# Optimization experiments

Hardware: AMD Instinct MI355X
Metric: run time of the kernel (lower is better)

Reference implementation:

```python
import jax, jax.numpy as jnp
import numpy as np

B, N, D_IN, H, NH = 8, 1024, 3072, 128, 4
DH = H // NH
LN_EPS = 1e-5


def make_mask(key, p):
    A = jax.random.bernoulli(key, p, (N, N)).astype(jnp.float32)
    A_tilde = A + jnp.eye(N, dtype=jnp.float32)  # add self-loops
    return jnp.where(A_tilde > 0, 0.0, -jnp.inf).astype(jnp.float32)


def setup_inputs() -> dict:
    key = jax.random.key(0)
    ks = jax.random.split(key, 20)
    s = 0.02
    inp = {
        "stim_features": jax.random.normal(ks[0], (B, D_IN), jnp.float32),
        # stim encoder
        "W_enc1": jax.random.normal(ks[1], (2 * H, D_IN), jnp.float32) * s,
        "b_enc1": jnp.zeros((2 * H,), jnp.float32),
        "ln_g": jnp.ones((2 * H,), jnp.float32),
        "ln_b": jnp.zeros((2 * H,), jnp.float32),
        "W_enc2": jax.random.normal(ks[2], (H, 2 * H), jnp.float32) * s,
        "b_enc2": jnp.zeros((H,), jnp.float32),
        "voxel_emb": jax.random.normal(ks[3], (N, H), jnp.float32) * 0.01,
        # GAT projection weights (Linear, no bias), [out, in]
        "W_func1": jax.random.normal(ks[4], (H, H), jnp.float32) * s,
        "W_roi1": jax.random.normal(ks[5], (H, H), jnp.float32) * s,
        "W_func2": jax.random.normal(ks[6], (H, H), jnp.float32) * s,
        "W_roi2": jax.random.normal(ks[7], (H, H), jnp.float32) * s,
        # fusion / skip / readout
        "W_fu1": jax.random.normal(ks[8], (H, 2 * H), jnp.float32) * s,
        "b_fu1": jnp.zeros((H,), jnp.float32),
        "W_fu2": jax.random.normal(ks[9], (H, 2 * H), jnp.float32) * s,
        "b_fu2": jnp.zeros((H,), jnp.float32),
        "W_sk1": jax.random.normal(ks[10], (H, H), jnp.float32) * s,
        "b_sk1": jnp.zeros((H,), jnp.float32),
        "W_sk2": jax.random.normal(ks[11], (H, H), jnp.float32) * s,
        "b_sk2": jnp.zeros((H,), jnp.float32),
        "W_ro": jax.random.normal(ks[12], (1, H), jnp.float32) * s,
        "b_ro": jnp.zeros((1,), jnp.float32),
        # static adjacency masks (buffers, 0 / -inf)
        "mask_func": make_mask(ks[13], 0.01),
        "mask_roi": make_mask(ks[14], 0.05),
    }
    return inp


def gat(h, W, mask):
    # h: [B, N, H]; W: [H, H]; mask: [N, N]
    Bq, Nq, _ = h.shape
    Wh = (h @ W.T).reshape(Bq, Nq, NH, DH).transpose(0, 2, 1, 3)  # [B, nh, N, dh]
    scores = jnp.einsum("bhnd,bhmd->bhnm", Wh, Wh) / np.sqrt(DH)
    scores = scores + mask[None, None]
    attn = jax.nn.softmax(scores, axis=-1)  # dropout = identity (eval mode)
    hp = jnp.einsum("bhnm,bhmd->bhnd", attn, Wh)
    hp = hp.transpose(0, 2, 1, 3).reshape(Bq, Nq, NH * DH)
    return jax.nn.elu(hp)


def reference(stim_features, W_enc1, b_enc1, ln_g, ln_b, W_enc2, b_enc2,
              voxel_emb, W_func1, W_roi1, W_func2, W_roi2,
              W_fu1, b_fu1, W_fu2, b_fu2, W_sk1, b_sk1, W_sk2, b_sk2,
              W_ro, b_ro, mask_func, mask_roi):
    # stim encoder: Linear -> LayerNorm -> GELU -> Linear (dropout = identity)
    z = stim_features @ W_enc1.T + b_enc1
    mu = jnp.mean(z, axis=-1, keepdims=True)
    var = jnp.var(z, axis=-1, keepdims=True)
    z = (z - mu) * jax.lax.rsqrt(var + LN_EPS) * ln_g + ln_b
    z = jax.nn.gelu(z, approximate=False)
    g = z @ W_enc2.T + b_enc2  # [B, H]

    x = g[:, None, :] + voxel_emb[None]  # [B, N, H]
    x_res1 = x
    h1 = jnp.concatenate([gat(x, W_func1, mask_func), gat(x, W_roi1, mask_roi)], axis=-1)
    x = h1 @ W_fu1.T + b_fu1
    x = x + (x_res1 @ W_sk1.T + b_sk1)
    x_res2 = x
    h2 = jnp.concatenate([gat(x, W_func2, mask_func), gat(x, W_roi2, mask_roi)], axis=-1)
    x = h2 @ W_fu2.T + b_fu2
    x = x + (x_res2 @ W_sk2.T + b_sk2)
    pred = (x @ W_ro.T + b_ro)[..., 0]  # [B, N]
    return pred
```

## Files before the change

kernel.cpp:

```cpp
#include <hip/hip_runtime.h>
#include <hip/hip_bf16.h>
#include <math.h>

#define B_SZ 8
#define N_SZ 1024
#define D_IN 3072
#define H_SZ 128
#define NH 4
#define DH 32
#define TWO_H 256
#define LN_EPS 1e-5f
#define CAP 128

typedef __attribute__((ext_vector_type(8))) short bf16x8;
typedef __attribute__((ext_vector_type(8))) unsigned short u16x8;
typedef __attribute__((ext_vector_type(4))) float f32x4;
typedef __attribute__((ext_vector_type(4))) unsigned int u32x4;

__device__ inline unsigned short f2bf(float f) {
    unsigned int u = __builtin_bit_cast(unsigned int, f);
    u += 0x7fffu + ((u >> 16) & 1u);
    return (unsigned short)(u >> 16);
}

__global__ __launch_bounds__(256) void prep_kernel(
        const float* __restrict__ Wfu1, const float* __restrict__ Wsk1,
        const float* __restrict__ Wfu2, const float* __restrict__ Wsk2,
        const float* __restrict__ Wf1, const float* __restrict__ Wr1,
        const float* __restrict__ Wf2, const float* __restrict__ Wr2,
        unsigned short* __restrict__ wb,
        const float* __restrict__ m0, const float* __restrict__ m1,
        int* __restrict__ i0, int* __restrict__ i1,
        int* __restrict__ d0, int* __restrict__ d1,
        const float* __restrict__ stim, const float* __restrict__ W1,
        const float* __restrict__ b1, float* __restrict__ z) {
    const int bid = blockIdx.x;
    const int tid = threadIdx.x;

    if (bid < 128) {
        const int j = bid;
        wb[j * 384 + tid] = f2bf(Wfu1[j * 256 + tid]);
        wb[49152 + j * 384 + tid] = f2bf(Wfu2[j * 256 + tid]);
        if (tid < 128) {
            wb[j * 384 + 256 + tid]         = f2bf(Wsk1[j * 128 + tid]);
            wb[49152 + j * 384 + 256 + tid] = f2bf(Wsk2[j * 128 + tid]);
            wb[98304  + j * 128 + tid] = f2bf(Wf1[j * 128 + tid]);
            wb[114688 + j * 128 + tid] = f2bf(Wr1[j * 128 + tid]);
            wb[131072 + j * 128 + tid] = f2bf(Wf2[j * 128 + tid]);
            wb[147456 + j * 128 + tid] = f2bf(Wr2[j * 128 + tid]);
        }
    } else if (bid < 640) {
        const int bIdx = bid - 128;
        const int gsel = bIdx >> 8;
        const float* mask = gsel ? m1 : m0;
        int* idx = gsel ? i1 : i0;
        int* deg = gsel ? d1 : d0;
        const int row = (bIdx & 255) * 4 + (tid >> 6);
        const int lane = tid & 63;
        const float* mrow = mask + (size_t)row * N_SZ;
        int* irow = idx + (size_t)row * CAP;

        int base = 0;
        #pragma unroll 4
        for (int t = 0; t < N_SZ / 64; ++t) {
            int c = t * 64 + lane;
            bool edge = (mrow[c] == 0.0f);
            unsigned long long ball = __ballot(edge);
            unsigned long long below = ball & ((1ull << lane) - 1ull);
            if (edge) {
                int p = base + __popcll(below);
                if (p < CAP) irow[p] = c;
            }
            base += __popcll(ball);
        }
        if (lane == 0) deg[row] = (base < CAP) ? base : CAP;
    } else {
        const int j = bid - 640;
        const float4* w4 = (const float4*)(W1 + (size_t)j * D_IN);
        const float4* s4 = (const float4*)stim;

        float acc[B_SZ];
        #pragma unroll
        for (int b = 0; b < B_SZ; ++b) acc[b] = 0.0f;

        #pragma unroll
        for (int i = 0; i < D_IN / 4 / 256; ++i) {
            const int k4 = tid + i * 256;
            const float4 w = w4[k4];
            #pragma unroll
            for (int b = 0; b < B_SZ; ++b) {
                const float4 s = s4[b * (D_IN / 4) + k4];
                acc[b] += s.x * w.x + s.y * w.y + s.z * w.z + s.w * w.w;
            }
        }
        #pragma unroll
        for (int b = 0; b < B_SZ; ++b) {
            float v = acc[b];
            v += __shfl_xor(v, 1);  v += __shfl_xor(v, 2);  v += __shfl_xor(v, 4);
            v += __shfl_xor(v, 8);  v += __shfl_xor(v, 16); v += __shfl_xor(v, 32);
            acc[b] = v;
        }
        __shared__ float red[4][B_SZ];
        const int wave = tid >> 6, lane = tid & 63;
        if (lane == 0) {
            #pragma unroll
            for (int b = 0; b < B_SZ; ++b) red[wave][b] = acc[b];
        }
        __syncthreads();
        if (tid < B_SZ) {
            float v = red[0][tid] + red[1][tid] + red[2][tid] + red[3][tid];
            z[tid * TWO_H + j] = v + b1[j];
        }
    }
}

__global__ __launch_bounds__(256) void enc23_kernel(
        const float* __restrict__ z,
        const float* __restrict__ lng, const float* __restrict__ lnb,
        const float* __restrict__ W2, const float* __restrict__ b2,
        float* __restrict__ g) {
    __shared__ float red[TWO_H];
    __shared__ float zgs[TWO_H];
    __shared__ float gp[2][H_SZ];
    const int b = blockIdx.x;
    const int tid = threadIdx.x;

    float zi = z[b * TWO_H + tid];
    red[tid] = zi; __syncthreads();
    for (int s = 128; s > 0; s >>= 1) { if (tid < s) red[tid] += red[tid + s]; __syncthreads(); }
    float mu = red[0] * (1.0f / TWO_H);
    __syncthreads();
    float dz = zi - mu;
    red[tid] = dz * dz; __syncthreads();
    for (int s = 128; s > 0; s >>= 1) { if (tid < s) red[tid] += red[tid + s]; __syncthreads(); }
    float var = red[0] * (1.0f / TWO_H);

    float zn = dz * (1.0f / sqrtf(var + LN_EPS)) * lng[tid] + lnb[tid];
    zgs[tid] = 0.5f * zn * (1.0f + erff(zn * 0.70710678118654752f));
    __syncthreads();

    const int j = tid & 127, half = tid >> 7;
    const float* w2r = W2 + (size_t)j * TWO_H + half * 128;
    const float* zh = &zgs[half * 128];
    float s = 0.0f;
    #pragma unroll 4
    for (int k = 0; k < 128; ++k) s += zh[k] * w2r[k];
    gp[half][j] = s;
    __syncthreads();
    if (tid < H_SZ) g[b * H_SZ + tid] = gp[0][tid] + gp[1][tid] + b2[tid];
}

template<int NSEG, bool OB16, bool AEMB, bool RO, bool AB16>
__global__ __launch_bounds__(256) void gemm_mfma(
        const void* __restrict__ a0, const void* __restrict__ a1,
        const void* __restrict__ a2,
        const float* __restrict__ gvec, const float* __restrict__ emb,
        const unsigned short* __restrict__ wba, const unsigned short* __restrict__ wbb,
        const float* __restrict__ bias1, const float* __restrict__ bias2,
        void* __restrict__ outa, void* __restrict__ outb,
        const float* __restrict__ Wro, const float* __restrict__ bro,
        float* __restrict__ pred) {
    const unsigned short* wb = blockIdx.y ? wbb : wba;
    void* out = blockIdx.y ? outb : outa;
    const int KW = NSEG * 128;

    __shared__ __align__(16) short As[32 * 128];
    __shared__ __align__(16) short Bs[64 * 128];
    __shared__ float part[2][32];

    const int bid = blockIdx.x;
    const int ct = bid & 1, rt = bid >> 1;
    const int row0 = rt * 32, col0 = ct * 64;
    const int tid = threadIdx.x;
    const int lane = tid & 63, w = tid >> 6;
    const int wm = w >> 1, wn = w & 1;
    const int lrow = lane & 15, lk = lane >> 4;

    f32x4 acc0 = {0.f, 0.f, 0.f, 0.f};
    f32x4 acc1 = {0.f, 0.f, 0.f, 0.f};

    for (int seg = 0; seg < NSEG; ++seg) {
        const void* src = (seg == 0) ? a0 : ((seg == 1) ? a1 : a2);
        const bool useEmb = AEMB && (NSEG == 1 || seg == 2);
        if (seg) __syncthreads();
        for (int gi = tid; gi < 512; gi += 256) {
            const int r = gi >> 4, kq = gi & 15;
            u16x8 t;
            if (useEmb) {
                const int row = row0 + r;
                const float4* gp = (const float4*)(gvec + (size_t)(row >> 10) * H_SZ) + kq * 2;
                const float4* ep = (const float4*)(emb + (size_t)(row & 1023) * H_SZ) + kq * 2;
                const float4 g0 = gp[0], g1 = gp[1], e0 = ep[0], e1 = ep[1];
                t[0] = f2bf(g0.x + e0.x); t[1] = f2bf(g0.y + e0.y);
                t[2] = f2bf(g0.z + e0.z); t[3] = f2bf(g0.w + e0.w);
                t[4] = f2bf(g1.x + e1.x); t[5] = f2bf(g1.y + e1.y);
                t[6] = f2bf(g1.z + e1.z); t[7] = f2bf(g1.w + e1.w);
            } else if (AB16) {
                t = *(const u16x8*)((const unsigned short*)src
                                    + (size_t)(row0 + r) * H_SZ + kq * 8);
            } else {
                const float4* sp = (const float4*)((const float*)src
                                    + (size_t)(row0 + r) * H_SZ) + kq * 2;
                const float4 v0 = sp[0], v1 = sp[1];
                t[0] = f2bf(v0.x); t[1] = f2bf(v0.y); t[2] = f2bf(v0.z); t[3] = f2bf(v0.w);
                t[4] = f2bf(v1.x); t[5] = f2bf(v1.y); t[6] = f2bf(v1.z); t[7] = f2bf(v1.w);
            }
            *(u16x8*)&As[r * 128 + ((kq * 8) ^ ((r & 7) << 3))] = t;
        }
        for (int gi = tid; gi < 1024; gi += 256) {
            const int c = gi >> 4, kq = gi & 15;
            const float4 v = *(const float4*)(wb + (size_t)(col0 + c) * KW + seg * 128 + kq * 8);
            *(float4*)&Bs[c * 128 + ((kq * 8) ^ ((c & 7) << 3))] = v;
        }
        __syncthreads();

        #pragma unroll
        for (int ks = 0; ks < 4; ++ks) {
            const int kof = ks * 32 + lk * 8;
            const int r = wm * 16 + lrow;
            const bf16x8 a = *(const bf16x8*)&As[r * 128 + (kof ^ ((r & 7) << 3))];
            const int c0 = wn * 32 + lrow;
            const bf16x8 b0 = *(const bf16x8*)&Bs[c0 * 128 + (kof ^ ((c0 & 7) << 3))];
            const int c1 = c0 + 16;
            const bf16x8 b1 = *(const bf16x8*)&Bs[c1 * 128 + (kof ^ ((c1 & 7) << 3))];
            acc0 = __builtin_amdgcn_mfma_f32_16x16x32_bf16(a, b0, acc0, 0, 0, 0);
            acc1 = __builtin_amdgcn_mfma_f32_16x16x32_bf16(a, b1, acc1, 0, 0, 0);
        }
    }

    const int rb = row0 + wm * 16 + lk * 4;
    if constexpr (RO) {
        float pr[4] = {0.f, 0.f, 0.f, 0.f};
        #pragma unroll
        for (int fc = 0; fc < 2; ++fc) {
            const int c = col0 + wn * 32 + fc * 16 + lrow;
            const float bias = bias1[c] + bias2[c];
            const float wro = Wro[c];
            const f32x4 a = fc ? acc1 : acc0;
            #pragma unroll
            for (int rr = 0; rr < 4; ++rr) pr[rr] += (a[rr] + bias) * wro;
        }
        #pragma unroll
        for (int rr = 0; rr < 4; ++rr) {
            pr[rr] += __shfl_xor(pr[rr], 1);
            pr[rr] += __shfl_xor(pr[rr], 2);
            pr[rr] += __shfl_xor(pr[rr], 4);
            pr[rr] += __shfl_xor(pr[rr], 8);
        }
        if (lrow == 0) {
            #pragma unroll
            for (int rr = 0; rr < 4; ++rr) part[wn][wm * 16 + lk * 4 + rr] = pr[rr];
        }
        __syncthreads();
        if (tid < 32) {
            float v = part[0][tid] + part[1][tid];
            if (ct == 0) v += bro[0];
            atomicAdd(pred + row0 + tid, v);
        }
    } else {
        #pragma unroll
        for (int fc = 0; fc < 2; ++fc) {
            const int c = col0 + wn * 32 + fc * 16 + lrow;
            const float bias = (bias1 ? bias1[c] : 0.0f) + (bias2 ? bias2[c] : 0.0f);
            const f32x4 a = fc ? acc1 : acc0;
            #pragma unroll
            for (int rr = 0; rr < 4; ++rr) {
                if constexpr (OB16) {
                    ((unsigned short*)out)[(size_t)(rb + rr) * H_SZ + c] = f2bf(a[rr] + bias);
                } else {
                    ((float*)out)[(size_t)(rb + rr) * H_SZ + c] = a[rr] + bias;
                }
            }
        }
    }
}

__global__ __launch_bounds__(256) void fusproj_kernel(
        const unsigned short* __restrict__ hf, const unsigned short* __restrict__ hr,
        const float* __restrict__ gvec, const float* __restrict__ emb,
        const unsigned short* __restrict__ wcat,
        const float* __restrict__ bfu, const float* __restrict__ bsk,
        const unsigned short* __restrict__ wpf, const unsigned short* __restrict__ wpr,
        unsigned short* __restrict__ x2, unsigned short* __restrict__ whf,
        unsigned short* __restrict__ whr) {
    __shared__ __align__(16) short As[16 * 128];
    __shared__ __align__(16) short Bs[128 * 128];
    const int row0 = blockIdx.x * 16;
    const int tid = threadIdx.x;
    const int lane = tid & 63, w = tid >> 6;
    const int lrow = lane & 15, lk = lane >> 4;

    f32x4 acc0 = {0.f, 0.f, 0.f, 0.f};
    f32x4 acc1 = {0.f, 0.f, 0.f, 0.f};

    for (int seg = 0; seg < 3; ++seg) {
        if (seg) __syncthreads();
        {
            const int r = tid >> 4, kq = tid & 15;
            u16x8 t;
            if (seg == 0) {
                t = *(const u16x8*)(hf + (size_t)(row0 + r) * H_SZ + kq * 8);
            } else if (seg == 1) {
                t = *(const u16x8*)(hr + (size_t)(row0 + r) * H_SZ + kq * 8);
            } else {
                const int row = row0 + r;
                const float4* gp = (const float4*)(gvec + (size_t)(row >> 10) * H_SZ) + kq * 2;
                const float4* ep = (const float4*)(emb + (size_t)(row & 1023) * H_SZ) + kq * 2;
                const float4 g0 = gp[0], g1 = gp[1], e0 = ep[0], e1 = ep[1];
                t[0] = f2bf(g0.x + e0.x); t[1] = f2bf(g0.y + e0.y);
                t[2] = f2bf(g0.z + e0.z); t[3] = f2bf(g0.w + e0.w);
                t[4] = f2bf(g1.x + e1.x); t[5] = f2bf(g1.y + e1.y);
                t[6] = f2bf(g1.z + e1.z); t[7] = f2bf(g1.w + e1.w);
            }
            *(u16x8*)&As[r * 128 + ((kq * 8) ^ ((r & 7) << 3))] = t;
        }
        for (int gi = tid; gi < 2048; gi += 256) {
            const int c = gi >> 4, kq = gi & 15;
            const float4 v = *(const float4*)(wcat + (size_t)c * 384 + seg * 128 + kq * 8);
            *(float4*)&Bs[c * 128 + ((kq * 8) ^ ((c & 7) << 3))] = v;
        }
        __syncthreads();

        #pragma unroll
        for (int ks = 0; ks < 4; ++ks) {
            const int kof = ks * 32 + lk * 8;
            const bf16x8 a = *(const bf16x8*)&As[lrow * 128 + (kof ^ ((lrow & 7) << 3))];
            const int c0 = w * 32 + lrow;
            const bf16x8 b0 = *(const bf16x8*)&Bs[c0 * 128 + (kof ^ ((c0 & 7) << 3))];
            const int c1 = c0 + 16;
            const bf16x8 b1 = *(const bf16x8*)&Bs[c1 * 128 + (kof ^ ((c1 & 7) << 3))];
            acc0 = __builtin_amdgcn_mfma_f32_16x16x32_bf16(a, b0, acc0, 0, 0, 0);
            acc1 = __builtin_amdgcn_mfma_f32_16x16x32_bf16(a, b1, acc1, 0, 0, 0);
        }
    }
    __syncthreads();

    const int rb = lk * 4;
    #pragma unroll
    for (int fc = 0; fc < 2; ++fc) {
        const int c = w * 32 + fc * 16 + lrow;
        const float bias = bfu[c] + bsk[c];
        const f32x4 a = fc ? acc1 : acc0;
        #pragma unroll
        for (int rr = 0; rr < 4; ++rr) {
            const unsigned short v = f2bf(a[rr] + bias);
            x2[(size_t)(row0 + rb + rr) * H_SZ + c] = v;
            const int rl = rb + rr;
            As[rl * 128 + (((c & ~7) ^ ((rl & 7) << 3)) | (c & 7))] = (short)v;
        }
    }
    __syncthreads();

    #pragma unroll
    for (int gsel = 0; gsel < 2; ++gsel) {
        const unsigned short* wp = gsel ? wpr : wpf;
        unsigned short* out = gsel ? whr : whf;
        if (gsel) __syncthreads();
        for (int gi = tid; gi < 2048; gi += 256) {
            const int c = gi >> 4, kq = gi & 15;
            const float4 v = *(const float4*)(wp + (size_t)c * 128 + kq * 8);
            *(float4*)&Bs[c * 128 + ((kq * 8) ^ ((c & 7) << 3))] = v;
        }
        __syncthreads();
        f32x4 p0 = {0.f, 0.f, 0.f, 0.f};
        f32x4 p1 = {0.f, 0.f, 0.f, 0.f};
        #pragma unroll
        for (int ks = 0; ks < 4; ++ks) {
            const int kof = ks * 32 + lk * 8;
            const bf16x8 a = *(const bf16x8*)&As[lrow * 128 + (kof ^ ((lrow & 7) << 3))];
            const int c0 = w * 32 + lrow;
            const bf16x8 b0 = *(const bf16x8*)&Bs[c0 * 128 + (kof ^ ((c0 & 7) << 3))];
            const int c1 = c0 + 16;
            const bf16x8 b1 = *(const bf16x8*)&Bs[c1 * 128 + (kof ^ ((c1 & 7) << 3))];
            p0 = __builtin_amdgcn_mfma_f32_16x16x32_bf16(a, b0, p0, 0, 0, 0);
            p1 = __builtin_amdgcn_mfma_f32_16x16x32_bf16(a, b1, p1, 0, 0, 0);
        }
        #pragma unroll
        for (int fc = 0; fc < 2; ++fc) {
            const int c = w * 32 + fc * 16 + lrow;
            const f32x4 a = fc ? p1 : p0;
            #pragma unroll
            for (int rr = 0; rr < 4; ++rr)
                out[(size_t)(row0 + rb + rr) * H_SZ + c] = f2bf(a[rr]);
        }
    }
}

__global__ __launch_bounds__(256) void fusro_kernel(
        const unsigned short* __restrict__ hf, const unsigned short* __restrict__ hr,
        const unsigned short* __restrict__ x2,
        const unsigned short* __restrict__ wcat,
        const float* __restrict__ bfu, const float* __restrict__ bsk,
        const float* __restrict__ Wro, const float* __restrict__ bro,
        float* __restrict__ pred) {
    __shared__ __align__(16) short As[16 * 128];
    __shared__ __align__(16) short Bs[128 * 128];
    __shared__ float part[4][16];
    const int row0 = blockIdx.x * 16;
    const int tid = threadIdx.x;
    const int lane = tid & 63, w = tid >> 6;
    const int lrow = lane & 15, lk = lane >> 4;

    f32x4 acc0 = {0.f, 0.f, 0.f, 0.f};
    f32x4 acc1 = {0.f, 0.f, 0.f, 0.f};

    for (int seg = 0; seg < 3; ++seg) {
        if (seg) __syncthreads();
        {
            const int r = tid >> 4, kq = tid & 15;
            const unsigned short* src = (seg == 0) ? hf : ((seg == 1) ? hr : x2);
            const u16x8 t = *(const u16x8*)(src + (size_t)(row0 + r) * H_SZ + kq * 8);
            *(u16x8*)&As[r * 128 + ((kq * 8) ^ ((r & 7) << 3))] = t;
        }
        for (int gi = tid; gi < 2048; gi += 256) {
            const int c = gi >> 4, kq = gi & 15;
            const float4 v = *(const float4*)(wcat + (size_t)c * 384 + seg * 128 + kq * 8);
            *(float4*)&Bs[c * 128 + ((kq * 8) ^ ((c & 7) << 3))] = v;
        }
        __syncthreads();

        #pragma unroll
        for (int ks = 0; ks < 4; ++ks) {
            const int kof = ks * 32 + lk * 8;
            const bf16x8 a = *(const bf16x8*)&As[lrow * 128 + (kof ^ ((lrow & 7) << 3))];
            const int c0 = w * 32 + lrow;
            const bf16x8 b0 = *(const bf16x8*)&Bs[c0 * 128 + (kof ^ ((c0 & 7) << 3))];
            const int c1 = c0 + 16;
            const bf16x8 b1 = *(const bf16x8*)&Bs[c1 * 128 + (kof ^ ((c1 & 7) << 3))];
            acc0 = __builtin_amdgcn_mfma_f32_16x16x32_bf16(a, b0, acc0, 0, 0, 0);
            acc1 = __builtin_amdgcn_mfma_f32_16x16x32_bf16(a, b1, acc1, 0, 0, 0);
        }
    }

    const int rb = lk * 4;
    float pr[4] = {0.f, 0.f, 0.f, 0.f};
    #pragma unroll
    for (int fc = 0; fc < 2; ++fc) {
        const int c = w * 32 + fc * 16 + lrow;
        const float bias = bfu[c] + bsk[c];
        const float wro = Wro[c];
        const f32x4 a = fc ? acc1 : acc0;
        #pragma unroll
        for (int rr = 0; rr < 4; ++rr) pr[rr] += (a[rr] + bias) * wro;
    }
    #pragma unroll
    for (int rr = 0; rr < 4; ++rr) {
        pr[rr] += __shfl_xor(pr[rr], 1);
        pr[rr] += __shfl_xor(pr[rr], 2);
        pr[rr] += __shfl_xor(pr[rr], 4);
        pr[rr] += __shfl_xor(pr[rr], 8);
    }
    if (lrow == 0) {
        #pragma unroll
        for (int rr = 0; rr < 4; ++rr) part[w][rb + rr] = pr[rr];
    }
    __syncthreads();
    if (tid < 16)
        pred[row0 + tid] = part[0][tid] + part[1][tid] + part[2][tid] + part[3][tid] + bro[0];
}

__global__ __launch_bounds__(256) void attn_kernel(
        const unsigned short* __restrict__ Wha, const unsigned short* __restrict__ Whb,
        const int* __restrict__ ia, const int* __restrict__ ib,
        const int* __restrict__ da, const int* __restrict__ db,
        unsigned short* __restrict__ oa, unsigned short* __restrict__ ob) {
    const unsigned short* Wh = blockIdx.y ? Whb : Wha;
    const int* idx = blockIdx.y ? ib : ia;
    const int* deg = blockIdx.y ? db : da;
    unsigned short* out = blockIdx.y ? ob : oa;

    const int bid = blockIdx.x;
    const int b = bid & 7;
    const int i = ((bid >> 3) << 2) | (threadIdx.x >> 6);
    const int bi = b * N_SZ + i;
    const int lane = threadIdx.x & 63;
    const int c = lane & 15;
    const int e4 = lane >> 4;

    const u32x4 qb = *(const u32x4*)(Wh + (size_t)bi * H_SZ + c * 8);
    float qf[8];
    #pragma unroll
    for (int m = 0; m < 4; ++m) {
        qf[2 * m]     = __builtin_bit_cast(float, qb[m] << 16) * 0.25505654741110714f;
        qf[2 * m + 1] = __builtin_bit_cast(float, qb[m] & 0xffff0000u) * 0.25505654741110714f;
    }

    const int dg = deg[i];
    const int* row = idx + (size_t)i * CAP;
    int idxv0 = row[lane] & 1023;
    int idxv1 = (dg > 64) ? (row[64 + lane] & 1023) : 0;

    const unsigned short* kbase = Wh + (size_t)b * N_SZ * H_SZ;

    float acc[8];
    #pragma unroll
    for (int k = 0; k < 8; ++k) acc[k] = 0.0f;
    float l = 0.0f;

    auto loadSeg = [&](int s, u32x4* kv) {
        const int srcv = (s >= 4) ? idxv1 : idxv0;
        const int off16 = (s & 3) << 4;
        #pragma unroll
        for (int t = 0; t < 4; ++t) {
            const int j0 = __builtin_amdgcn_readlane(srcv, off16 + 4 * t);
            const int j1 = __builtin_amdgcn_readlane(srcv, off16 + 4 * t + 1);
            const int j2 = __builtin_amdgcn_readlane(srcv, off16 + 4 * t + 2);
            const int j3 = __builtin_amdgcn_readlane(srcv, off16 + 4 * t + 3);
            const int jlo = (e4 & 1) ? j1 : j0;
            const int jhi = (e4 & 1) ? j3 : j2;
            const int j = (e4 & 2) ? jhi : jlo;
            kv[t] = *(const u32x4*)(kbase + (size_t)j * H_SZ + c * 8);
        }
    };
    auto computeSeg = [&](int s, const u32x4* kv) {
        const int ebase = s << 4;
        #pragma unroll
        for (int t = 0; t < 4; ++t) {
            float kf[8];
            #pragma unroll
            for (int m = 0; m < 4; ++m) {
                kf[2 * m]     = __builtin_bit_cast(float, kv[t][m] << 16);
                kf[2 * m + 1] = __builtin_bit_cast(float, kv[t][m] & 0xffff0000u);
            }
            float s2 = 0.0f;
            #pragma unroll
            for (int k = 0; k < 8; ++k) s2 += qf[k] * kf[k];
            s2 += __shfl_xor(s2, 1);
            s2 += __shfl_xor(s2, 2);
            const bool valid = (ebase + 4 * t + e4) < dg;
            const float p = valid ? __builtin_amdgcn_exp2f(s2) : 0.0f;
            l += p;
            #pragma unroll
            for (int k = 0; k < 8; ++k) acc[k] += p * kf[k];
        }
    };

    const int nseg = (dg + 15) >> 4;
    u32x4 kvA[4], kvB[4];
    loadSeg(0, kvA);
    int seg = 0;
    while (true) {
        if (seg + 1 < nseg) loadSeg(seg + 1, kvB);
        computeSeg(seg, kvA);
        ++seg; if (seg >= nseg) break;
        if (seg + 1 < nseg) loadSeg(seg + 1, kvA);
        computeSeg(seg, kvB);
        ++seg; if (seg >= nseg) break;
    }

    l += __shfl_xor(l, 16);
    l += __shfl_xor(l, 32);
    #pragma unroll
    for (int k = 0; k < 8; ++k) {
        acc[k] += __shfl_xor(acc[k], 16);
        acc[k] += __shfl_xor(acc[k], 32);
    }

    if (e4 == 0) {
        const float inv = 1.0f / l;
        u16x8 ov;
        #pragma unroll
        for (int k = 0; k < 8; ++k) {
            const float hp = acc[k] * inv;
            const float o = (hp > 0.0f) ? hp
                 : (__builtin_amdgcn_exp2f(hp * 1.4426950408889634f) - 1.0f);
            ov[k] = f2bf(o);
        }
        *(u16x8*)(out + (size_t)bi * H_SZ + c * 8) = ov;
    }
}

extern "C" void kernel_launch(void* const* d_in, const int* in_sizes, int n_in,
                              void* d_out, int out_size, void* d_ws, size_t ws_size,
                              hipStream_t stream) {
    const float* stim   = (const float*)d_in[0];
    const float* W_enc1 = (const float*)d_in[1];
    const float* b_enc1 = (const float*)d_in[2];
    const float* ln_g   = (const float*)d_in[3];
    const float* ln_b   = (const float*)d_in[4];
    const float* W_enc2 = (const float*)d_in[5];
    const float* b_enc2 = (const float*)d_in[6];
    const float* vox    = (const float*)d_in[7];
    const float* W_f1   = (const float*)d_in[8];
    const float* W_r1   = (const float*)d_in[9];
    const float* W_f2   = (const float*)d_in[10];
    const float* W_r2   = (const float*)d_in[11];
    const float* W_fu1  = (const float*)d_in[12];
    const float* b_fu1  = (const float*)d_in[13];
    const float* W_fu2  = (const float*)d_in[14];
    const float* b_fu2  = (const float*)d_in[15];
    const float* W_sk1  = (const float*)d_in[16];
    const float* b_sk1  = (const float*)d_in[17];
    const float* W_sk2  = (const float*)d_in[18];
    const float* b_sk2  = (const float*)d_in[19];
    const float* W_ro   = (const float*)d_in[20];
    const float* b_ro   = (const float*)d_in[21];
    const float* mask_f = (const float*)d_in[22];
    const float* mask_r = (const float*)d_in[23];

    float* pred = (float*)d_out;

    float* ws  = (float*)d_ws;
    float* z   = ws;
    float* g   = z + 2048;
    unsigned short* x2_16 = (unsigned short*)(g + 1024);
    unsigned short* hf16  = x2_16 + 1048576;
    unsigned short* hr16  = hf16 + 1048576;
    unsigned short* Whf16 = hr16 + 1048576;
    unsigned short* Whr16 = Whf16 + 1048576;
    int* idxf  = (int*)(Whr16 + 1048576);
    int* idxr  = idxf + N_SZ * CAP;
    int* degf  = idxr + N_SZ * CAP;
    int* degr  = degf + N_SZ;
    unsigned short* wb16 = (unsigned short*)(degr + N_SZ);
    unsigned short* wcat1 = wb16;
    unsigned short* wcat2 = wb16 + 49152;
    unsigned short* wpf1  = wb16 + 98304;
    unsigned short* wpr1  = wb16 + 114688;
    unsigned short* wpf2  = wb16 + 131072;
    unsigned short* wpr2  = wb16 + 147456;

    const int BN = B_SZ * N_SZ;

    prep_kernel<<<896, 256, 0, stream>>>(
        W_fu1, W_sk1, W_fu2, W_sk2, W_f1, W_r1, W_f2, W_r2, wb16,
        mask_f, mask_r, idxf, idxr, degf, degr,
        stim, W_enc1, b_enc1, z);
    enc23_kernel<<<B_SZ, 256, 0, stream>>>(z, ln_g, ln_b, W_enc2, b_enc2, g);

    gemm_mfma<1, true, true, false, false><<<dim3(BN / 32 * 2, 2), 256, 0, stream>>>(
        nullptr, nullptr, nullptr, g, vox, wpf1, wpr1, nullptr, nullptr,
        Whf16, Whr16, nullptr, nullptr, nullptr);
    attn_kernel<<<dim3(BN / 4, 2), 256, 0, stream>>>(Whf16, Whr16, idxf, idxr, degf, degr,
                                                     hf16, hr16);
    fusproj_kernel<<<BN / 16, 256, 0, stream>>>(
        hf16, hr16, g, vox, wcat1, b_fu1, b_sk1, wpf2, wpr2,
        x2_16, Whf16, Whr16);

    attn_kernel<<<dim3(BN / 4, 2), 256, 0, stream>>>(Whf16, Whr16, idxf, idxr, degf, degr,
                                                     hf16, hr16);
    fusro_kernel<<<BN / 16, 256, 0, stream>>>(
        hf16, hr16, x2_16, wcat2, b_fu2, b_sk2, W_ro, b_ro, pred);
}
```

Measured before the change: 88.21 us.

## Double row tile in fusion kernels, skip padded neighbor loads, simplify gemm template

The fusproj and fusro kernels now process 32 rows per block instead of 16. Each wave computes two 16-row MFMA tiles against the same B fragments, so each 128x128 weight tile staged in shared memory is reused over twice as many rows and half as many blocks are launched. The attention kernel now skips neighbor gathers and compute for 4-element groups past the node degree in the final segment, avoiding wasted loads. The generic gemm template also drops its unused multi-segment, bias and readout paths. Halving the block count lowers parallelism and raises register use per wave.

```diff
diff --git a/kernel.cpp b/kernel.cpp
--- a/kernel.cpp
+++ b/kernel.cpp
@@ -150,23 +150,18 @@
     if (tid < H_SZ) g[b * H_SZ + tid] = gp[0][tid] + gp[1][tid] + b2[tid];
 }
 
-template<int NSEG, bool OB16, bool AEMB, bool RO, bool AB16>
+template<int NSEG, bool AEMB, bool AB16>
 __global__ __launch_bounds__(256) void gemm_mfma(
-        const void* __restrict__ a0, const void* __restrict__ a1,
-        const void* __restrict__ a2,
+        const void* __restrict__ a0,
         const float* __restrict__ gvec, const float* __restrict__ emb,
         const unsigned short* __restrict__ wba, const unsigned short* __restrict__ wbb,
-        const float* __restrict__ bias1, const float* __restrict__ bias2,
-        void* __restrict__ outa, void* __restrict__ outb,
-        const float* __restrict__ Wro, const float* __restrict__ bro,
-        float* __restrict__ pred) {
+        void* __restrict__ outa, void* __restrict__ outb) {
     const unsigned short* wb = blockIdx.y ? wbb : wba;
     void* out = blockIdx.y ? outb : outa;
     const int KW = NSEG * 128;
 
     __shared__ __align__(16) short As[32 * 128];
     __shared__ __align__(16) short Bs[64 * 128];
-    __shared__ float part[2][32];
 
     const int bid = blockIdx.x;
     const int ct = bid & 1, rt = bid >> 1;
@@ -180,13 +175,11 @@
     f32x4 acc1 = {0.f, 0.f, 0.f, 0.f};
 
     for (int seg = 0; seg < NSEG; ++seg) {
-        const void* src = (seg == 0) ? a0 : ((seg == 1) ? a1 : a2);
-        const bool useEmb = AEMB && (NSEG == 1 || seg == 2);
         if (seg) __syncthreads();
         for (int gi = tid; gi < 512; gi += 256) {
             const int r = gi >> 4, kq = gi & 15;
             u16x8 t;
-            if (useEmb) {
+            if (AEMB) {
                 const int row = row0 + r;
                 const float4* gp = (const float4*)(gvec + (size_t)(row >> 10) * H_SZ) + kq * 2;
                 const float4* ep = (const float4*)(emb + (size_t)(row & 1023) * H_SZ) + kq * 2;
@@ -196,10 +189,10 @@
                 t[4] = f2bf(g1.x + e1.x); t[5] = f2bf(g1.y + e1.y);
                 t[6] = f2bf(g1.z + e1.z); t[7] = f2bf(g1.w + e1.w);
             } else if (AB16) {
-                t = *(const u16x8*)((const unsigned short*)src
+                t = *(const u16x8*)((const unsigned short*)a0
                                     + (size_t)(row0 + r) * H_SZ + kq * 8);
             } else {
-                const float4* sp = (const float4*)((const float*)src
+                const float4* sp = (const float4*)((const float*)a0
                                     + (size_t)(row0 + r) * H_SZ) + kq * 2;
                 const float4 v0 = sp[0], v1 = sp[1];
                 t[0] = f2bf(v0.x); t[1] = f2bf(v0.y); t[2] = f2bf(v0.z); t[3] = f2bf(v0.w);
@@ -229,49 +222,13 @@
     }
 
     const int rb = row0 + wm * 16 + lk * 4;
-    if constexpr (RO) {
-        float pr[4] = {0.f, 0.f, 0.f, 0.f};
-        #pragma unroll
-        for (int fc = 0; fc < 2; ++fc) {
-            const int c = col0 + wn * 32 + fc * 16 + lrow;
-            const float bias = bias1[c] + bias2[c];
-            const float wro = Wro[c];
-            const f32x4 a = fc ? acc1 : acc0;
-            #pragma unroll
-            for (int rr = 0; rr < 4; ++rr) pr[rr] += (a[rr] + bias) * wro;
-        }
-        #pragma unroll
-        for (int rr = 0; rr < 4; ++rr) {
-            pr[rr] += __shfl_xor(pr[rr], 1);
-            pr[rr] += __shfl_xor(pr[rr], 2);
-            pr[rr] += __shfl_xor(pr[rr], 4);
-            pr[rr] += __shfl_xor(pr[rr], 8);
-        }
-        if (lrow == 0) {
-            #pragma unroll
-            for (int rr = 0; rr < 4; ++rr) part[wn][wm * 16 + lk * 4 + rr] = pr[rr];
-        }
-        __syncthreads();
-        if (tid < 32) {
-            float v = part[0][tid] + part[1][tid];
-            if (ct == 0) v += bro[0];
-            atomicAdd(pred + row0 + tid, v);
-        }
-    } else {
-        #pragma unroll
-        for (int fc = 0; fc < 2; ++fc) {
-            const int c = col0 + wn * 32 + fc * 16 + lrow;
-            const float bias = (bias1 ? bias1[c] : 0.0f) + (bias2 ? bias2[c] : 0.0f);
-            const f32x4 a = fc ? acc1 : acc0;
-            #pragma unroll
-            for (int rr = 0; rr < 4; ++rr) {
-                if constexpr (OB16) {
-                    ((unsigned short*)out)[(size_t)(rb + rr) * H_SZ + c] = f2bf(a[rr] + bias);
-                } else {
-                    ((float*)out)[(size_t)(rb + rr) * H_SZ + c] = a[rr] + bias;
-                }
-            }
-        }
+    #pragma unroll
+    for (int fc = 0; fc < 2; ++fc) {
+        const int c = col0 + wn * 32 + fc * 16 + lrow;
+        const f32x4 a = fc ? acc1 : acc0;
+        #pragma unroll
+        for (int rr = 0; rr < 4; ++rr)
+            ((unsigned short*)out)[(size_t)(rb + rr) * H_SZ + c] = f2bf(a[rr]);
     }
 }
 
@@ -283,20 +240,20 @@
         const unsigned short* __restrict__ wpf, const unsigned short* __restrict__ wpr,
         unsigned short* __restrict__ x2, unsigned short* __restrict__ whf,
         unsigned short* __restrict__ whr) {
-    __shared__ __align__(16) short As[16 * 128];
+    __shared__ __align__(16) short As[32 * 128];
     __shared__ __align__(16) short Bs[128 * 128];
-    const int row0 = blockIdx.x * 16;
+    const int row0 = blockIdx.x * 32;
     const int tid = threadIdx.x;
     const int lane = tid & 63, w = tid >> 6;
     const int lrow = lane & 15, lk = lane >> 4;
 
-    f32x4 acc0 = {0.f, 0.f, 0.f, 0.f};
-    f32x4 acc1 = {0.f, 0.f, 0.f, 0.f};
+    f32x4 acc[2][2] = {{{0.f,0.f,0.f,0.f},{0.f,0.f,0.f,0.f}},
+                       {{0.f,0.f,0.f,0.f},{0.f,0.f,0.f,0.f}}};
 
     for (int seg = 0; seg < 3; ++seg) {
         if (seg) __syncthreads();
-        {
-            const int r = tid >> 4, kq = tid & 15;
+        for (int gi = tid; gi < 512; gi += 256) {
+            const int r = gi >> 4, kq = gi & 15;
             u16x8 t;
             if (seg == 0) {
                 t = *(const u16x8*)(hf + (size_t)(row0 + r) * H_SZ + kq * 8);
@@ -324,29 +281,35 @@
         #pragma unroll
         for (int ks = 0; ks < 4; ++ks) {
             const int kof = ks * 32 + lk * 8;
-            const bf16x8 a = *(const bf16x8*)&As[lrow * 128 + (kof ^ ((lrow & 7) << 3))];
-            const int c0 = w * 32 + lrow;
+            const int c0 = w * 32 + lrow, c1 = c0 + 16;
             const bf16x8 b0 = *(const bf16x8*)&Bs[c0 * 128 + (kof ^ ((c0 & 7) << 3))];
-            const int c1 = c0 + 16;
             const bf16x8 b1 = *(const bf16x8*)&Bs[c1 * 128 + (kof ^ ((c1 & 7) << 3))];
-            acc0 = __builtin_amdgcn_mfma_f32_16x16x32_bf16(a, b0, acc0, 0, 0, 0);
-            acc1 = __builtin_amdgcn_mfma_f32_16x16x32_bf16(a, b1, acc1, 0, 0, 0);
+            #pragma unroll
+            for (int m = 0; m < 2; ++m) {
+                const int r = m * 16 + lrow;
+                const bf16x8 a = *(const bf16x8*)&As[r * 128 + (kof ^ ((r & 7) << 3))];
+                acc[m][0] = __builtin_amdgcn_mfma_f32_16x16x32_bf16(a, b0, acc[m][0], 0, 0, 0);
+                acc[m][1] = __builtin_amdgcn_mfma_f32_16x16x32_bf16(a, b1, acc[m][1], 0, 0, 0);
+            }
         }
     }
     __syncthreads();
 
-    const int rb = lk * 4;
     #pragma unroll
-    for (int fc = 0; fc < 2; ++fc) {
-        const int c = w * 32 + fc * 16 + lrow;
-        const float bias = bfu[c] + bsk[c];
-        const f32x4 a = fc ? acc1 : acc0;
-        #pragma unroll
-        for (int rr = 0; rr < 4; ++rr) {
-            const unsigned short v = f2bf(a[rr] + bias);
-            x2[(size_t)(row0 + rb + rr) * H_SZ + c] = v;
-            const int rl = rb + rr;
-            As[rl * 128 + (((c & ~7) ^ ((rl & 7) << 3)) | (c & 7))] = (short)v;
+    for (int m = 0; m < 2; ++m) {
+        const int rb = m * 16 + lk * 4;
+        #pragma unroll
+        for (int fc = 0; fc < 2; ++fc) {
+            const int c = w * 32 + fc * 16 + lrow;
+            const float bias = bfu[c] + bsk[c];
+            const f32x4 a = acc[m][fc];
+            #pragma unroll
+            for (int rr = 0; rr < 4; ++rr) {
+                const unsigned short v = f2bf(a[rr] + bias);
+                x2[(size_t)(row0 + rb + rr) * H_SZ + c] = v;
+                const int rl = rb + rr;
+                As[rl * 128 + (((c & ~7) ^ ((rl & 7) << 3)) | (c & 7))] = (short)v;
+            }
         }
     }
     __syncthreads();
@@ -362,26 +325,33 @@
             *(float4*)&Bs[c * 128 + ((kq * 8) ^ ((c & 7) << 3))] = v;
         }
         __syncthreads();
-        f32x4 p0 = {0.f, 0.f, 0.f, 0.f};
-        f32x4 p1 = {0.f, 0.f, 0.f, 0.f};
+        f32x4 p[2][2] = {{{0.f,0.f,0.f,0.f},{0.f,0.f,0.f,0.f}},
+                         {{0.f,0.f,0.f,0.f},{0.f,0.f,0.f,0.f}}};
         #pragma unroll
         for (int ks = 0; ks < 4; ++ks) {
             const int kof = ks * 32 + lk * 8;
-            const bf16x8 a = *(const bf16x8*)&As[lrow * 128 + (kof ^ ((lrow & 7) << 3))];
-            const int c0 = w * 32 + lrow;
+            const int c0 = w * 32 + lrow, c1 = c0 + 16;
             const bf16x8 b0 = *(const bf16x8*)&Bs[c0 * 128 + (kof ^ ((c0 & 7) << 3))];
-            const int c1 = c0 + 16;
             const bf16x8 b1 = *(const bf16x8*)&Bs[c1 * 128 + (kof ^ ((c1 & 7) << 3))];
-            p0 = __builtin_amdgcn_mfma_f32_16x16x32_bf16(a, b0, p0, 0, 0, 0);
-            p1 = __builtin_amdgcn_mfma_f32_16x16x32_bf16(a, b1, p1, 0, 0, 0);
-        }
-        #pragma unroll
-        for (int fc = 0; fc < 2; ++fc) {
-            const int c = w * 32 + fc * 16 + lrow;
-            const f32x4 a = fc ? p1 : p0;
-            #pragma unroll
-            for (int rr = 0; rr < 4; ++rr)
-                out[(size_t)(row0 + rb + rr) * H_SZ + c] = f2bf(a[rr]);
+            #pragma unroll
+            for (int m = 0; m < 2; ++m) {
+                const int r = m * 16 + lrow;
+                const bf16x8 a = *(const bf16x8*)&As[r * 128 + (kof ^ ((r & 7) << 3))];
+                p[m][0] = __builtin_amdgcn_mfma_f32_16x16x32_bf16(a, b0, p[m][0], 0, 0, 0);
+                p[m][1] = __builtin_amdgcn_mfma_f32_16x16x32_bf16(a, b1, p[m][1], 0, 0, 0);
+            }
+        }
+        #pragma unroll
+        for (int m = 0; m < 2; ++m) {
+            const int rb = m * 16 + lk * 4;
+            #pragma unroll
+            for (int fc = 0; fc < 2; ++fc) {
+                const int c = w * 32 + fc * 16 + lrow;
+                const f32x4 a = p[m][fc];
+                #pragma unroll
+                for (int rr = 0; rr < 4; ++rr)
+                    out[(size_t)(row0 + rb + rr) * H_SZ + c] = f2bf(a[rr]);
+            }
         }
     }
 }
@@ -393,21 +363,21 @@
         const float* __restrict__ bfu, const float* __restrict__ bsk,
         const float* __restrict__ Wro, const float* __restrict__ bro,
         float* __restrict__ pred) {
-    __shared__ __align__(16) short As[16 * 128];
+    __shared__ __align__(16) short As[32 * 128];
     __shared__ __align__(16) short Bs[128 * 128];
-    __shared__ float part[4][16];
-    const int row0 = blockIdx.x * 16;
+    __shared__ float part[4][32];
+    const int row0 = blockIdx.x * 32;
     const int tid = threadIdx.x;
     const int lane = tid & 63, w = tid >> 6;
     const int lrow = lane & 15, lk = lane >> 4;
 
-    f32x4 acc0 = {0.f, 0.f, 0.f, 0.f};
-    f32x4 acc1 = {0.f, 0.f, 0.f, 0.f};
+    f32x4 acc[2][2] = {{{0.f,0.f,0.f,0.f},{0.f,0.f,0.f,0.f}},
+                       {{0.f,0.f,0.f,0.f},{0.f,0.f,0.f,0.f}}};
 
     for (int seg = 0; seg < 3; ++seg) {
         if (seg) __syncthreads();
-        {
-            const int r = tid >> 4, kq = tid & 15;
+        for (int gi = tid; gi < 512; gi += 256) {
+            const int r = gi >> 4, kq = gi & 15;
             const unsigned short* src = (seg == 0) ? hf : ((seg == 1) ? hr : x2);
             const u16x8 t = *(const u16x8*)(src + (size_t)(row0 + r) * H_SZ + kq * 8);
             *(u16x8*)&As[r * 128 + ((kq * 8) ^ ((r & 7) << 3))] = t;
@@ -422,40 +392,46 @@
         #pragma unroll
         for (int ks = 0; ks < 4; ++ks) {
             const int kof = ks * 32 + lk * 8;
-            const bf16x8 a = *(const bf16x8*)&As[lrow * 128 + (kof ^ ((lrow & 7) << 3))];
-            const int c0 = w * 32 + lrow;
+            const int c0 = w * 32 + lrow, c1 = c0 + 16;
             const bf16x8 b0 = *(const bf16x8*)&Bs[c0 * 128 + (kof ^ ((c0 & 7) << 3))];
-            const int c1 = c0 + 16;
             const bf16x8 b1 = *(const bf16x8*)&Bs[c1 * 128 + (kof ^ ((c1 & 7) << 3))];
-            acc0 = __builtin_amdgcn_mfma_f32_16x16x32_bf16(a, b0, acc0, 0, 0, 0);
-            acc1 = __builtin_amdgcn_mfma_f32_16x16x32_bf16(a, b1, acc1, 0, 0, 0);
-        }
-    }
-
-    const int rb = lk * 4;
-    float pr[4] = {0.f, 0.f, 0.f, 0.f};
+            #pragma unroll
+            for (int m = 0; m < 2; ++m) {
+                const int r = m * 16 + lrow;
+                const bf16x8 a = *(const bf16x8*)&As[r * 128 + (kof ^ ((r & 7) << 3))];
+                acc[m][0] = __builtin_amdgcn_mfma_f32_16x16x32_bf16(a, b0, acc[m][0], 0, 0, 0);
+                acc[m][1] = __builtin_amdgcn_mfma_f32_16x16x32_bf16(a, b1, acc[m][1], 0, 0, 0);
+            }
+        }
+    }
+
     #pragma unroll
-    for (int fc = 0; fc < 2; ++fc) {
-        const int c = w * 32 + fc * 16 + lrow;
-        const float bias = bfu[c] + bsk[c];
-        const float wro = Wro[c];
-        const f32x4 a = fc ? acc1 : acc0;
-        #pragma unroll
-        for (int rr = 0; rr < 4; ++rr) pr[rr] += (a[rr] + bias) * wro;
-    }
-    #pragma unroll
-    for (int rr = 0; rr < 4; ++rr) {
-        pr[rr] += __shfl_xor(pr[rr], 1);
-        pr[rr] += __shfl_xor(pr[rr], 2);
-        pr[rr] += __shfl_xor(pr[rr], 4);
-        pr[rr] += __shfl_xor(pr[rr], 8);
-    }
-    if (lrow == 0) {
-        #pragma unroll
-        for (int rr = 0; rr < 4; ++rr) part[w][rb + rr] = pr[rr];
+    for (int m = 0; m < 2; ++m) {
+        const int rb = m * 16 + lk * 4;
+        float pr[4] = {0.f, 0.f, 0.f, 0.f};
+        #pragma unroll
+        for (int fc = 0; fc < 2; ++fc) {
+            const int c = w * 32 + fc * 16 + lrow;
+            const float bias = bfu[c] + bsk[c];
+            const float wro = Wro[c];
+            const f32x4 a = acc[m][fc];
+            #pragma unroll
+            for (int rr = 0; rr < 4; ++rr) pr[rr] += (a[rr] + bias) * wro;
+        }
+        #pragma unroll
+        for (int rr = 0; rr < 4; ++rr) {
+            pr[rr] += __shfl_xor(pr[rr], 1);
+            pr[rr] += __shfl_xor(pr[rr], 2);
+            pr[rr] += __shfl_xor(pr[rr], 4);
+            pr[rr] += __shfl_xor(pr[rr], 8);
+        }
+        if (lrow == 0) {
+            #pragma unroll
+            for (int rr = 0; rr < 4; ++rr) part[w][rb + rr] = pr[rr];
+        }
     }
     __syncthreads();
-    if (tid < 16)
+    if (tid < 32)
         pred[row0 + tid] = part[0][tid] + part[1][tid] + part[2][tid] + part[3][tid] + bro[0];
 }
 
@@ -500,38 +476,44 @@
     auto loadSeg = [&](int s, u32x4* kv) {
         const int srcv = (s >= 4) ? idxv1 : idxv0;
         const int off16 = (s & 3) << 4;
+        const int cnt = dg - (s << 4);
         #pragma unroll
         for (int t = 0; t < 4; ++t) {
-            const int j0 = __builtin_amdgcn_readlane(srcv, off16 + 4 * t);
-            const int j1 = __builtin_amdgcn_readlane(srcv, off16 + 4 * t + 1);
-            const int j2 = __builtin_amdgcn_readlane(srcv, off16 + 4 * t + 2);
-            const int j3 = __builtin_amdgcn_readlane(srcv, off16 + 4 * t + 3);
-            const int jlo = (e4 & 1) ? j1 : j0;
-            const int jhi = (e4 & 1) ? j3 : j2;
-            const int j = (e4 & 2) ? jhi : jlo;
-            kv[t] = *(const u32x4*)(kbase + (size_t)j * H_SZ + c * 8);
+            if (4 * t < cnt) {
+                const int j0 = __builtin_amdgcn_readlane(srcv, off16 + 4 * t);
+                const int j1 = __builtin_amdgcn_readlane(srcv, off16 + 4 * t + 1);
+                const int j2 = __builtin_amdgcn_readlane(srcv, off16 + 4 * t + 2);
+                const int j3 = __builtin_amdgcn_readlane(srcv, off16 + 4 * t + 3);
+                const int jlo = (e4 & 1) ? j1 : j0;
+                const int jhi = (e4 & 1) ? j3 : j2;
+                const int j = (e4 & 2) ? jhi : jlo;
+                kv[t] = *(const u32x4*)(kbase + (size_t)j * H_SZ + c * 8);
+            }
         }
     };
     auto computeSeg = [&](int s, const u32x4* kv) {
         const int ebase = s << 4;
+        const int cnt = dg - ebase;
         #pragma unroll
         for (int t = 0; t < 4; ++t) {
-            float kf[8];
-            #pragma unroll
-            for (int m = 0; m < 4; ++m) {
-                kf[2 * m]     = __builtin_bit_cast(float, kv[t][m] << 16);
-                kf[2 * m + 1] = __builtin_bit_cast(float, kv[t][m] & 0xffff0000u);
-            }
-            float s2 = 0.0f;
-            #pragma unroll
-            for (int k = 0; k < 8; ++k) s2 += qf[k] * kf[k];
-            s2 += __shfl_xor(s2, 1);
-            s2 += __shfl_xor(s2, 2);
-            const bool valid = (ebase + 4 * t + e4) < dg;
-            const float p = valid ? __builtin_amdgcn_exp2f(s2) : 0.0f;
-            l += p;
-            #pragma unroll
-            for (int k = 0; k < 8; ++k) acc[k] += p * kf[k];
+            if (4 * t < cnt) {
+                float kf[8];
+                #pragma unroll
+                for (int m = 0; m < 4; ++m) {
+                    kf[2 * m]     = __builtin_bit_cast(float, kv[t][m] << 16);
+                    kf[2 * m + 1] = __builtin_bit_cast(float, kv[t][m] & 0xffff0000u);
+                }
+                float s2 = 0.0f;
+                #pragma unroll
+                for (int k = 0; k < 8; ++k) s2 += qf[k] * kf[k];
+                s2 += __shfl_xor(s2, 1);
+                s2 += __shfl_xor(s2, 2);
+                const bool valid = (ebase + 4 * t + e4) < dg;
+                const float p = valid ? __builtin_amdgcn_exp2f(s2) : 0.0f;
+                l += p;
+                #pragma unroll
+                for (int k = 0; k < 8; ++k) acc[k] += p * kf[k];
+            }
         }
     };
 
@@ -628,17 +610,16 @@
         stim, W_enc1, b_enc1, z);
     enc23_kernel<<<B_SZ, 256, 0, stream>>>(z, ln_g, ln_b, W_enc2, b_enc2, g);
 
-    gemm_mfma<1, true, true, false, false><<<dim3(BN / 32 * 2, 2), 256, 0, stream>>>(
-        nullptr, nullptr, nullptr, g, vox, wpf1, wpr1, nullptr, nullptr,
-        Whf16, Whr16, nullptr, nullptr, nullptr);
+    gemm_mfma<1, true, false><<<dim3(BN / 32 * 2, 2), 256, 0, stream>>>(
+        nullptr, g, vox, wpf1, wpr1, Whf16, Whr16);
     attn_kernel<<<dim3(BN / 4, 2), 256, 0, stream>>>(Whf16, Whr16, idxf, idxr, degf, degr,
                                                      hf16, hr16);
-    fusproj_kernel<<<BN / 16, 256, 0, stream>>>(
+    fusproj_kernel<<<BN / 32, 256, 0, stream>>>(
         hf16, hr16, g, vox, wcat1, b_fu1, b_sk1, wpf2, wpr2,
         x2_16, Whf16, Whr16);
 
     attn_kernel<<<dim3(BN / 4, 2), 256, 0, stream>>>(Whf16, Whr16, idxf, idxr, degf, degr,
                                                      hf16, hr16);
-    fusro_kernel<<<BN / 16, 256, 0, stream>>>(
+    fusro_kernel<<<BN / 32, 256, 0, stream>>>(
         hf16, hr16, x2_16, wcat2, b_fu2, b_sk2, W_ro, b_ro, pred);
 }
```

After: 95.12 us. 7.8% more time.
